# Kernel tuning notes

Measured on AMD Instinct MI355X. Metric: run time of the kernel, lower is better.

The kernel has to match this reference:

```python
import jax, jax.numpy as jnp
import numpy as np

B, OBS, ACT, NT, E, H1, H2, D = 4096, 390, 20, 10, 8, 1024, 512, 256


def setup_inputs() -> dict:
    key = jax.random.key(0)
    ks = jax.random.split(key, 16)
    f32 = jnp.float32

    def w(k, shape, fan_in):
        return jax.random.normal(k, shape, f32) / np.float32(np.sqrt(fan_in))

    return {
        "state_feat": jax.random.normal(ks[0], (B, OBS), f32),
        "act": jax.random.normal(ks[1], (B, ACT), f32),
        "task_id": jax.random.randint(ks[2], (B,), 0, NT, jnp.int32),
        "rep_W1": w(ks[3], (OBS + ACT, H1), OBS + ACT),
        "rep_b1": jnp.zeros((H1,), f32),
        "rep_W2": w(ks[4], (H1, H1), H1),
        "rep_b2": jnp.zeros((H1,), f32),
        "emb": 0.5 * jax.random.normal(ks[5], (NT, D), f32),
        "kW1": w(ks[6], (E, H1, H2), H1),
        "kb1": jnp.zeros((E, H2), f32),
        "kW2": w(ks[7], (E, H2, D), H2),
        "kb2": jnp.zeros((E, D), f32),
        "vW1": w(ks[8], (E, H1, H2), H1),
        "vb1": jnp.zeros((E, H2), f32),
        "vW2": w(ks[9], (E, H2, D), H2),
        "vb2": jnp.zeros((E, D), f32),
        "tW1": w(ks[10], (D, D), D),
        "tb1": jnp.zeros((D,), f32),
        "tW2": w(ks[11], (D, D), D),
        "tb2": jnp.zeros((D,), f32),
        "tW3": w(ks[12], (D, 1), D),
        "tb3": jnp.zeros((1,), f32),
    }


def reference(state_feat, act, task_id, rep_W1, rep_b1, rep_W2, rep_b2, emb,
              kW1, kb1, kW2, kb2, vW1, vb1, vW2, vb2,
              tW1, tb1, tW2, tb2, tW3, tb3):
    # representation: mlp([obs+act, 1024, 1024]) -> ReLU on first layer only
    x = jnp.concatenate([state_feat, act], axis=-1)              # [B, 410]
    rep = jnp.maximum(x @ rep_W1 + rep_b1, 0.0) @ rep_W2 + rep_b2  # [B, H1]
    query = jnp.tanh(emb[task_id])                               # [B, D]

    # batched per-expert key/value MLPs (grouped GEMM instead of python loop)
    hk = jnp.maximum(jnp.einsum('bi,eio->ebo', rep, kW1) + kb1[:, None, :], 0.0)
    keys = jnp.einsum('ebo,eod->ebd', hk, kW2) + kb2[:, None, :]   # [E, B, D]
    hv = jnp.maximum(jnp.einsum('bi,eio->ebo', rep, vW1) + vb1[:, None, :], 0.0)
    vals = jnp.einsum('ebo,eod->ebd', hv, vW2) + vb2[:, None, :]   # [E, B, D]

    scores = jnp.einsum('bd,ebd->be', query, keys)               # [B, E]
    weight = jax.nn.softmax(scores, axis=1)                      # [B, E]
    tower_in = jnp.einsum('be,ebd->bd', weight, vals)            # [B, D]

    # tower: mlp([256, 256, 256, 1]) -> ReLU, ReLU, Identity
    h = jnp.maximum(tower_in @ tW1 + tb1, 0.0)
    h = jnp.maximum(h @ tW2 + tb2, 0.0)
    q = (h @ tW3 + tb3)[:, 0]                                    # [B]

    expert_loss = -jnp.mean(
        jnp.sum(jnp.clip(jnp.log(weight + 1e-10), -6.0, 0.0), axis=-1) * 0.3)
    return q, expert_loss
```

## Files before the change

### kernel.cpp

```cpp
#include <hip/hip_runtime.h>

constexpr int Bn   = 4096;
constexpr int OBS  = 390;
constexpr int ACTN = 20;
constexpr int IN   = 410;
constexpr int KPAD = 416;
constexpr int E    = 8;
constexpr int NT   = 10;
constexpr int H1   = 1024;
constexpr int H2   = 512;
constexpr int D    = 256;

typedef __bf16 bf16x8 __attribute__((ext_vector_type(8)));
typedef float  f32x4  __attribute__((ext_vector_type(4)));

__device__ __forceinline__ unsigned short f2bf(float f) {
    unsigned int u = __float_as_uint(f);
    unsigned int r = u + 0x7fffu + ((u >> 16) & 1u);
    return (unsigned short)(r >> 16);
}
__device__ __forceinline__ float bf2f(unsigned short h) {
    return __uint_as_float(((unsigned int)h) << 16);
}
__device__ __forceinline__ void gload16(void* lds_dst, const void* g_src) {
    __builtin_amdgcn_global_load_lds(
        (const __attribute__((address_space(1))) void*)g_src,
        (__attribute__((address_space(3))) void*)lds_dst,
        16, 0, 0);
}

__global__ void prep_kernel(const float* __restrict__ sf, const float* __restrict__ ac,
                            unsigned short* __restrict__ x) {
    int idx = blockIdx.x * blockDim.x + threadIdx.x;
    if (idx >= Bn * KPAD) return;
    int b = idx / KPAD;
    int k = idx - b * KPAD;
    float v = 0.f;
    if (k < OBS) v = sf[b * OBS + k];
    else if (k < IN) v = ac[b * ACTN + (k - OBS)];
    x[idx] = f2bf(v);
}

__global__ __launch_bounds__(256) void qproj_kernel(
    const float* __restrict__ kW2, const float* __restrict__ kb2,
    const float* __restrict__ emb, float* __restrict__ qp, float* __restrict__ qb)
{
    __shared__ float tq[NT][D];
    for (int i = threadIdx.x; i < NT * D; i += 256)
        tq[i / D][i - (i / D) * D] = tanhf(emb[i]);
    __syncthreads();

    if (blockIdx.x < 16) {
        int e = blockIdx.x >> 1;
        int h = (blockIdx.x & 1) * 256 + threadIdx.x;
        const float4* row = (const float4*)(kW2 + ((long long)e * H2 + h) * D);
        float acc[NT] = {};
        for (int d4 = 0; d4 < D / 4; ++d4) {
            float4 wv = row[d4];
#pragma unroll
            for (int t = 0; t < NT; ++t)
                acc[t] += wv.x * tq[t][d4 * 4] + wv.y * tq[t][d4 * 4 + 1]
                        + wv.z * tq[t][d4 * 4 + 2] + wv.w * tq[t][d4 * 4 + 3];
        }
#pragma unroll
        for (int t = 0; t < NT; ++t)
            qp[((long long)e * NT + t) * H2 + h] = acc[t];
    } else {
        if (threadIdx.x < E * NT) {
            int e = threadIdx.x / NT, t = threadIdx.x - e * NT;
            float s = 0.f;
            for (int d = 0; d < D; ++d) s += kb2[e * D + d] * tq[t][d];
            qb[e * NT + t] = s;
        }
    }
}

struct TDesc {
    const float* W;
    unsigned short* WT;
    int K, N, Kpad;
    long long gsW, gsO;
    int tilesX, tilesY, perG;
    int start;
};
struct TDescArr { TDesc d[8]; };

__global__ __launch_bounds__(256) void mega_transpose(TDescArr da) {
    int bid = blockIdx.x;
    int i = 0;
#pragma unroll
    for (int j = 1; j < 8; ++j) if (bid >= da.d[j].start) i = j;
    TDesc dd = da.d[i];
    int local = bid - dd.start;
    int g   = local / dd.perG;
    int rem = local - g * dd.perG;
    int tyt = rem / dd.tilesX;
    int txt = rem - tyt * dd.tilesX;
    const float* W = dd.W + (long long)g * dd.gsW;
    unsigned short* WT = dd.WT + (long long)g * dd.gsO;

    __shared__ float tile[32][33];
    int tx = threadIdx.x & 31, ty = threadIdx.x >> 5;
    int k0 = tyt * 32, n0 = txt * 32;
#pragma unroll
    for (int r = 0; r < 4; ++r) {
        int k = k0 + ty + r * 8;
        tile[ty + r * 8][tx] = (k < dd.K) ? W[(long long)k * dd.N + n0 + tx] : 0.f;
    }
    __syncthreads();
#pragma unroll
    for (int r = 0; r < 4; ++r) {
        int n = n0 + ty + r * 8;
        WT[(long long)n * dd.Kpad + k0 + tx] = f2bf(tile[tx][ty + r * 8]);
    }
}

__global__ void bias_concat(const float* __restrict__ kb1, const float* __restrict__ vb1,
                            float* __restrict__ b1cat) {
    int i = blockIdx.x * blockDim.x + threadIdx.x;
    if (i < E * H2)          b1cat[i] = kb1[i];
    else if (i < 2 * E * H2) b1cat[i] = vb1[i - E * H2];
}

template <int ACTF, int OUTF, int BK>
__global__ __launch_bounds__(256) void gemm_bf16(
    const unsigned short* __restrict__ A, const unsigned short* __restrict__ BT,
    const float* __restrict__ bias, void* __restrict__ Cout,
    int K, int ldc,
    long long gsA, long long gsBT, long long gsBias, long long gsC)
{
    constexpr int CH   = BK / 8;
    constexpr int RPR  = 256 / CH;
    constexpr int RNDS = 128 / RPR;
    constexpr int TB   = 128 * BK * 2;
    constexpr int RS   = CH * 16;

    const int g = blockIdx.z;
    A    += (long long)g * gsA;
    BT   += (long long)g * gsBT;
    bias += (long long)g * gsBias;
    float*          Cf = (float*)Cout + (long long)g * gsC;
    unsigned short* Cb = (unsigned short*)Cout + (long long)g * gsC;

    __shared__ alignas(16) char smem[2 * TB];
    const int t  = threadIdx.x;
    const int w  = t >> 6, l = t & 63;
    const int lr = l & 15, lk = l >> 4;
    const int gm = blockIdx.y * 128, gn = blockIdx.x * 128;
    const int wm = (w >> 1) * 64,   wn = (w & 1) * 64;

    const int srow = t / CH;
    const int swzS = (CH == 8) ? (srow & 7) : ((srow >> 1) & 3);
    const int sc   = (t % CH) ^ swzS;
    const unsigned short* gA = A  + (long long)(gm + srow) * K + sc * 8;
    const unsigned short* gB = BT + (long long)(gn + srow) * K + sc * 8;

    const int swzL = (CH == 8) ? (lr & 7) : ((lr >> 1) & 3);
    const int aoff = (wm + lr) * RS + ((lk ^ swzL) * 16);
    const int boff = TB + (wn + lr) * RS + ((lk ^ swzL) * 16);

    f32x4 acc[4][4] = {};

    for (int k0 = 0; k0 < K; k0 += BK) {
#pragma unroll
        for (int j = 0; j < RNDS; ++j) {
            gload16(smem + j * 4096 + w * 1024,      gA + k0 + (long long)j * RPR * K);
            gload16(smem + TB + j * 4096 + w * 1024, gB + k0 + (long long)j * RPR * K);
        }
        __syncthreads();

        bf16x8 af[4], bfr[4];
#pragma unroll
        for (int i = 0; i < 4; ++i) {
            af[i]  = *(const bf16x8*)(smem + aoff + i * 16 * RS);
            bfr[i] = *(const bf16x8*)(smem + boff + i * 16 * RS);
        }
#pragma unroll
        for (int mi = 0; mi < 4; ++mi)
#pragma unroll
            for (int ni = 0; ni < 4; ++ni)
                acc[mi][ni] = __builtin_amdgcn_mfma_f32_16x16x32_bf16(
                    af[mi], bfr[ni], acc[mi][ni], 0, 0, 0);

        if constexpr (BK == 64) {
#pragma unroll
            for (int i = 0; i < 4; ++i) {
                af[i]  = *(const bf16x8*)(smem + (aoff ^ 64) + i * 16 * RS);
                bfr[i] = *(const bf16x8*)(smem + (boff ^ 64) + i * 16 * RS);
            }
#pragma unroll
            for (int mi = 0; mi < 4; ++mi)
#pragma unroll
                for (int ni = 0; ni < 4; ++ni)
                    acc[mi][ni] = __builtin_amdgcn_mfma_f32_16x16x32_bf16(
                        af[mi], bfr[ni], acc[mi][ni], 0, 0, 0);
        }
        __syncthreads();
    }

    const int orow0 = gm + wm + lk * 4;
    const int ocol0 = gn + wn + lr;
    float bv[4];
#pragma unroll
    for (int ni = 0; ni < 4; ++ni) bv[ni] = bias[gn + wn + lr + ni * 16];
#pragma unroll
    for (int mi = 0; mi < 4; ++mi)
#pragma unroll
        for (int ni = 0; ni < 4; ++ni)
#pragma unroll
            for (int r = 0; r < 4; ++r) {
                float v = acc[mi][ni][r] + bv[ni];
                if (ACTF == 1) v = fmaxf(v, 0.f);
                long long off = (long long)(orow0 + mi * 16 + r) * ldc + ocol0 + ni * 16;
                if (OUTF == 0) Cf[off] = v;
                else           Cb[off] = f2bf(v);
            }
}

template <int KTOT, int ACTF, int OUTF>
__global__ __launch_bounds__(512, 2) void gemm256(
    const unsigned short* __restrict__ A, const unsigned short* __restrict__ BT,
    const float* __restrict__ bias, void* __restrict__ Cout,
    int ldc, long long gsA, long long gsBT, long long gsBias, long long gsC)
{
    constexpr int NT_ = KTOT / 64;
    static_assert(NT_ >= 4 && (NT_ % 2) == 0, "KTOT must be multiple of 128");

    const int g = blockIdx.z;
    A    += (long long)g * gsA;
    BT   += (long long)g * gsBT;
    bias += (long long)g * gsBias;
    float*          Cf = (float*)Cout + (long long)g * gsC;
    unsigned short* Cb = (unsigned short*)Cout + (long long)g * gsC;

    __shared__ __align__(16) char smem[131072];

    const int tid = threadIdx.x;
    const int l  = tid & 63;
    const int lr = l & 15, lk = l >> 4;
    const int w  = tid >> 6;
    const int wr = w >> 2, wc = w & 3;
    const int gm = blockIdx.y * 256, gn = blockIdx.x * 256;

    const int srow = tid >> 3;
    const int cg   = (tid & 7) ^ (srow & 7);
    const unsigned short* gA = A  + (long long)(gm + srow) * KTOT + cg * 8;
    const unsigned short* gB = BT + (long long)(gn + srow) * KTOT + cg * 8;
    const int wbase = (tid & ~63) * 16;

    const int cs0 = ((0 | lk) ^ (lr & 7)) * 16;
    const int cs1 = ((4 | lk) ^ (lr & 7)) * 16;
    const int aRow = wr * 16384 + lr * 128;
    const int bRow = 32768 + (wc >> 1) * 16384 + ((wc & 1) * 64 + lr) * 128;

    f32x4 acc[8][4] = {};

    auto stA = [&](int c, int s, int kt) {
        const unsigned short* src = gA + (long long)(s * 128) * KTOT + kt * 64;
        char* d = smem + c * 65536 + s * 16384 + wbase;
        gload16(d,        src);
        gload16(d + 8192, src + (long long)64 * KTOT);
    };
    auto stB = [&](int c, int s, int kt) {
        const unsigned short* src = gB + (long long)(s * 128) * KTOT + kt * 64;
        char* d = smem + c * 65536 + 32768 + s * 16384 + wbase;
        gload16(d,        src);
        gload16(d + 8192, src + (long long)64 * KTOT);
    };

    stA(0, 0, 0); stA(0, 1, 0); stB(0, 0, 0); stB(0, 1, 0);
    stA(1, 0, 1); stA(1, 1, 1);
    asm volatile("s_waitcnt vmcnt(4)" ::: "memory");
    __builtin_amdgcn_s_barrier();
    __builtin_amdgcn_sched_barrier(0);

#pragma unroll
    for (int kt = 0; kt < NT_; ++kt) {
        const int c = kt & 1;
        const char* bufc = smem + c * 65536;
        bf16x8 a0[4], a1[4], b0[4], b1[4];

#pragma unroll
        for (int m = 0; m < 4; ++m) {
            const char* base = bufc + aRow + m * (16 * 128);
            a0[m] = *(const bf16x8*)(base + cs0);
            a1[m] = *(const bf16x8*)(base + cs1);
        }
#pragma unroll
        for (int n = 0; n < 4; ++n) {
            const char* base = bufc + bRow + n * (16 * 128);
            b0[n] = *(const bf16x8*)(base + cs0);
            b1[n] = *(const bf16x8*)(base + cs1);
        }
        if (kt + 1 < NT_) { stB(c ^ 1, 0, kt + 1); stB(c ^ 1, 1, kt + 1); }
        __builtin_amdgcn_s_setprio(1);
#pragma unroll
        for (int m = 0; m < 4; ++m)
#pragma unroll
            for (int n = 0; n < 4; ++n) {
                acc[m][n] = __builtin_amdgcn_mfma_f32_16x16x32_bf16(a0[m], b0[n], acc[m][n], 0, 0, 0);
                acc[m][n] = __builtin_amdgcn_mfma_f32_16x16x32_bf16(a1[m], b1[n], acc[m][n], 0, 0, 0);
            }
        __builtin_amdgcn_s_setprio(0);

#pragma unroll
        for (int m = 0; m < 4; ++m) {
            const char* base = bufc + aRow + (64 + m * 16) * 128;
            a0[m] = *(const bf16x8*)(base + cs0);
            a1[m] = *(const bf16x8*)(base + cs1);
        }
        asm volatile("s_waitcnt lgkmcnt(0)" ::: "memory");
        __builtin_amdgcn_sched_barrier(0);
        if (kt + 2 < NT_) {
            __builtin_amdgcn_s_barrier();
            __builtin_amdgcn_sched_barrier(0);
            stA(c, 0, kt + 2); stA(c, 1, kt + 2);
        }
        __builtin_amdgcn_s_setprio(1);
#pragma unroll
        for (int m = 0; m < 4; ++m)
#pragma unroll
            for (int n = 0; n < 4; ++n) {
                acc[4 + m][n] = __builtin_amdgcn_mfma_f32_16x16x32_bf16(a0[m], b0[n], acc[4 + m][n], 0, 0, 0);
                acc[4 + m][n] = __builtin_amdgcn_mfma_f32_16x16x32_bf16(a1[m], b1[n], acc[4 + m][n], 0, 0, 0);
            }
        __builtin_amdgcn_s_setprio(0);

        if (kt + 1 < NT_) {
            if (kt + 2 < NT_) { asm volatile("s_waitcnt vmcnt(4)" ::: "memory"); }
            else              { asm volatile("s_waitcnt vmcnt(0)" ::: "memory"); }
            __builtin_amdgcn_sched_barrier(0);
            __builtin_amdgcn_s_barrier();
            __builtin_amdgcn_sched_barrier(0);
        }
    }

    const int orow0 = gm + wr * 128 + lk * 4;
    const int ocol0 = gn + wc * 64 + lr;
    float bv[4];
#pragma unroll
    for (int ni = 0; ni < 4; ++ni) bv[ni] = bias[gn + wc * 64 + lr + ni * 16];
#pragma unroll
    for (int mi = 0; mi < 8; ++mi)
#pragma unroll
        for (int ni = 0; ni < 4; ++ni)
#pragma unroll
            for (int r = 0; r < 4; ++r) {
                float v = acc[mi][ni][r] + bv[ni];
                if (ACTF == 1) v = fmaxf(v, 0.f);
                long long off = (long long)(orow0 + mi * 16 + r) * ldc + ocol0 + ni * 16;
                if (OUTF == 0) Cf[off] = v;
                else           Cb[off] = f2bf(v);
            }
}

__global__ __launch_bounds__(256) void attn_score_kernel(
    const unsigned short* __restrict__ hk, const unsigned short* __restrict__ vals,
    const float* __restrict__ qp, const float* __restrict__ qb,
    const int* __restrict__ task_id, unsigned short* __restrict__ tower_in,
    float* __restrict__ loss_partial)
{
    int wv   = threadIdx.x >> 6;
    int lane = threadIdx.x & 63;
    int b    = blockIdx.x * 4 + wv;
    int t    = task_id[b];

    float s[E];
#pragma unroll
    for (int e = 0; e < E; ++e) {
        const ushort4 h4a = *(const ushort4*)&hk[((long long)e * Bn + b) * H2 + lane * 8];
        const ushort4 h4b = *(const ushort4*)&hk[((long long)e * Bn + b) * H2 + lane * 8 + 4];
        const float4 q4a = *(const float4*)&qp[((long long)e * NT + t) * H2 + lane * 8];
        const float4 q4b = *(const float4*)&qp[((long long)e * NT + t) * H2 + lane * 8 + 4];
        float p = bf2f(h4a.x) * q4a.x + bf2f(h4a.y) * q4a.y
                + bf2f(h4a.z) * q4a.z + bf2f(h4a.w) * q4a.w
                + bf2f(h4b.x) * q4b.x + bf2f(h4b.y) * q4b.y
                + bf2f(h4b.z) * q4b.z + bf2f(h4b.w) * q4b.w;
#pragma unroll
        for (int off = 32; off > 0; off >>= 1) p += __shfl_xor(p, off, 64);
        s[e] = p + qb[e * NT + t];
    }

    float m = s[0];
#pragma unroll
    for (int e = 1; e < E; ++e) m = fmaxf(m, s[e]);
    float wgt[E];
    float sum = 0.f;
#pragma unroll
    for (int e = 0; e < E; ++e) { wgt[e] = expf(s[e] - m); sum += wgt[e]; }
    float inv = 1.f / sum;

    int d0 = lane * 4;
    float4 acc = make_float4(0.f, 0.f, 0.f, 0.f);
    float lb = 0.f;
#pragma unroll
    for (int e = 0; e < E; ++e) {
        float we = wgt[e] * inv;
        uint2 vv = *(const uint2*)&vals[((long long)e * Bn + b) * D + d0];
        acc.x += we * __uint_as_float(vv.x << 16);
        acc.y += we * __uint_as_float(vv.x & 0xffff0000u);
        acc.z += we * __uint_as_float(vv.y << 16);
        acc.w += we * __uint_as_float(vv.y & 0xffff0000u);
        lb += fminf(fmaxf(logf(we + 1e-10f), -6.f), 0.f);
    }
    ushort4 o;
    o.x = f2bf(acc.x); o.y = f2bf(acc.y); o.z = f2bf(acc.z); o.w = f2bf(acc.w);
    *(ushort4*)&tower_in[(long long)b * D + d0] = o;

    __shared__ float sm[4];
    if (lane == 0) sm[wv] = lb;
    __syncthreads();
    if (threadIdx.x == 0)
        loss_partial[blockIdx.x] = sm[0] + sm[1] + sm[2] + sm[3];
}

__global__ __launch_bounds__(256) void qdot_loss_kernel(
    const float* __restrict__ t2, const float* __restrict__ tW3,
    const float* __restrict__ tb3, float* __restrict__ out,
    const float* __restrict__ lossp)
{
    if (blockIdx.x == Bn / 4) {
        float s = 0.f;
        for (int i = threadIdx.x; i < Bn / 4; i += 256) s += lossp[i];
#pragma unroll
        for (int off = 32; off > 0; off >>= 1) s += __shfl_xor(s, off, 64);
        __shared__ float sm[4];
        if ((threadIdx.x & 63) == 0) sm[threadIdx.x >> 6] = s;
        __syncthreads();
        if (threadIdx.x == 0) out[Bn] = (-0.3f / Bn) * (sm[0] + sm[1] + sm[2] + sm[3]);
        return;
    }
    int wv   = threadIdx.x >> 6;
    int lane = threadIdx.x & 63;
    int b    = blockIdx.x * 4 + wv;
    int d0   = lane * 4;
    float4 h4 = *(const float4*)&t2[(long long)b * D + d0];
    float4 w4 = *(const float4*)&tW3[d0];
    float p = h4.x * w4.x + h4.y * w4.y + h4.z * w4.z + h4.w * w4.w;
#pragma unroll
    for (int off = 32; off > 0; off >>= 1) p += __shfl_xor(p, off, 64);
    if (lane == 0) out[b] = p + tb3[0];
}

extern "C" void kernel_launch(void* const* d_in, const int* in_sizes, int n_in,
                              void* d_out, int out_size, void* d_ws, size_t ws_size,
                              hipStream_t stream) {
    const float* state_feat = (const float*)d_in[0];
    const float* act        = (const float*)d_in[1];
    const int*   task_id    = (const int*)d_in[2];
    const float* rep_W1 = (const float*)d_in[3];
    const float* rep_b1 = (const float*)d_in[4];
    const float* rep_W2 = (const float*)d_in[5];
    const float* rep_b2 = (const float*)d_in[6];
    const float* emb    = (const float*)d_in[7];
    const float* kW1 = (const float*)d_in[8];
    const float* kb1 = (const float*)d_in[9];
    const float* kW2 = (const float*)d_in[10];
    const float* kb2 = (const float*)d_in[11];
    const float* vW1 = (const float*)d_in[12];
    const float* vb1 = (const float*)d_in[13];
    const float* vW2 = (const float*)d_in[14];
    const float* vb2 = (const float*)d_in[15];
    const float* tW1 = (const float*)d_in[16];
    const float* tb1 = (const float*)d_in[17];
    const float* tW2 = (const float*)d_in[18];
    const float* tb2 = (const float*)d_in[19];
    const float* tW3 = (const float*)d_in[20];
    const float* tb3 = (const float*)d_in[21];
    float* out = (float*)d_out;

    char* p = (char*)d_ws;
    auto alloc = [&](size_t bytes) {
        char* r = p;
        p += (bytes + 255) & ~(size_t)255;
        return r;
    };
    unsigned short* x      = (unsigned short*)alloc((size_t)Bn * KPAD * 2);
    unsigned short* repW1T = (unsigned short*)alloc((size_t)H1 * KPAD * 2);
    unsigned short* repW2T = (unsigned short*)alloc((size_t)H1 * H1 * 2);
    unsigned short* w1T    = (unsigned short*)alloc((size_t)2 * E * H2 * H1 * 2);
    unsigned short* w2T    = (unsigned short*)alloc((size_t)E * D * H2 * 2);
    unsigned short* tW1T   = (unsigned short*)alloc((size_t)D * D * 2);
    unsigned short* tW2T   = (unsigned short*)alloc((size_t)D * D * 2);
    float*          b1cat  = (float*)alloc((size_t)2 * E * H2 * 4);
    float*          qp     = (float*)alloc((size_t)E * NT * H2 * 4);
    float*          qb     = (float*)alloc((size_t)E * NT * 4);
    char*           h1zone = alloc((size_t)Bn * H1 * 2);
    unsigned short* rep    = (unsigned short*)alloc((size_t)Bn * H1 * 2);
    unsigned short* hkv    = (unsigned short*)alloc((size_t)2 * E * Bn * H2 * 2);
    unsigned short* vals   = (unsigned short*)alloc((size_t)E * Bn * D * 2);
    float*          lossp  = (float*)alloc((size_t)(Bn / 4) * 4);

    unsigned short* h1       = (unsigned short*)h1zone;
    unsigned short* tower_in = (unsigned short*)h1zone;
    unsigned short* t1       = (unsigned short*)(h1zone + (size_t)Bn * D * 2);
    float*          t2       = (float*)(h1zone + (size_t)2 * Bn * D * 2);
    unsigned short* hk = hkv;
    unsigned short* hv = hkv + (size_t)E * Bn * H2;

    TDescArr da;
    int startAcc = 0;
    auto setd = [&](int i, const float* W, unsigned short* WT, int K, int N, int Kpad,
                    long long gsW, long long gsO, int groups) {
        TDesc& dd = da.d[i];
        dd.W = W; dd.WT = WT; dd.K = K; dd.N = N; dd.Kpad = Kpad;
        dd.gsW = gsW; dd.gsO = gsO;
        dd.tilesX = N / 32; dd.tilesY = Kpad / 32;
        dd.perG = dd.tilesX * dd.tilesY;
        dd.start = startAcc;
        startAcc += dd.perG * groups;
    };
    setd(0, rep_W1, repW1T, IN, H1, KPAD, 0, 0, 1);
    setd(1, rep_W2, repW2T, H1, H1, H1, 0, 0, 1);
    setd(2, kW1, w1T,                       H1, H2, H1, (long long)H1 * H2, (long long)H2 * H1, E);
    setd(3, vW1, w1T + (size_t)E * H2 * H1, H1, H2, H1, (long long)H1 * H2, (long long)H2 * H1, E);
    setd(4, vW2, w2T,                       H2, D, H2, (long long)H2 * D, (long long)D * H2, E);
    setd(5, tW1, tW1T, D, D, D, 0, 0, 1);
    setd(6, tW2, tW2T, D, D, D, 0, 0, 1);
    da.d[7] = da.d[6];
    da.d[7].start = 0x7fffffff;
    mega_transpose<<<startAcc, 256, 0, stream>>>(da);

    bias_concat<<<(2 * E * H2) / 256, 256, 0, stream>>>(kb1, vb1, b1cat);
    prep_kernel<<<(Bn * KPAD + 255) / 256, 256, 0, stream>>>(state_feat, act, x);
    qproj_kernel<<<17, 256, 0, stream>>>(kW2, kb2, emb, qp, qb);

    gemm_bf16<1, 1, 32><<<dim3(H1 / 128, Bn / 128, 1), 256, 0, stream>>>(
        x, repW1T, rep_b1, h1, KPAD, H1, 0, 0, 0, 0);
    gemm_bf16<0, 1, 64><<<dim3(H1 / 128, Bn / 128, 1), 256, 0, stream>>>(
        h1, repW2T, rep_b2, rep, H1, H1, 0, 0, 0, 0);

    gemm256<H1, 1, 1><<<dim3(H2 / 256, Bn / 256, 2 * E), 512, 0, stream>>>(
        rep, w1T, b1cat, hkv, H2,
        0, (long long)H2 * H1, H2, (long long)Bn * H2);
    gemm_bf16<0, 1, 64><<<dim3(D / 128, Bn / 128, E), 256, 0, stream>>>(
        hv, w2T, vb2, vals, H2, D,
        (long long)Bn * H2, (long long)D * H2, D, (long long)Bn * D);

    attn_score_kernel<<<Bn / 4, 256, 0, stream>>>(
        hk, vals, qp, qb, task_id, tower_in, lossp);

    gemm_bf16<1, 1, 64><<<dim3(D / 128, Bn / 128, 1), 256, 0, stream>>>(
        tower_in, tW1T, tb1, t1, D, D, 0, 0, 0, 0);
    gemm_bf16<1, 0, 64><<<dim3(D / 128, Bn / 128, 1), 256, 0, stream>>>(
        t1, tW2T, tb2, t2, D, D, 0, 0, 0, 0);

    qdot_loss_kernel<<<Bn / 4 + 1, 256, 0, stream>>>(t2, tW3, tb3, out, lossp);
}
```

Baseline: 188.4 us.

## Fuse key-score dot into expert GEMM epilogue, merge prep kernels, widen transpose

The expert layer-1 GEMM epilogue now dots the ReLU'd key hidden activations with the projected query for each row's task. It writes per-block partial scores to a small buffer instead of storing the bf16 hidden keys, and the attention kernel just sums these partials. This removes the write and re-read of the hk activations. The three small setup kernels are merged into one launch, and weight transposes use 64x64 tiles with float4 loads and 16-byte bf16 stores. In exchange the epilogue does extra gathered qp loads and shuffles, and scores are now computed from fp32 rather than bf16-rounded activations.

```diff
diff --git a/kernel.cpp b/kernel.cpp
--- a/kernel.cpp
+++ b/kernel.cpp
@@ -13,6 +13,7 @@
 
 typedef __bf16 bf16x8 __attribute__((ext_vector_type(8)));
 typedef float  f32x4  __attribute__((ext_vector_type(4)));
+typedef unsigned short u16x8 __attribute__((ext_vector_type(8)));
 
 __device__ __forceinline__ unsigned short f2bf(float f) {
     unsigned int u = __float_as_uint(f);
@@ -29,97 +30,110 @@
         16, 0, 0);
 }
 
-__global__ void prep_kernel(const float* __restrict__ sf, const float* __restrict__ ac,
-                            unsigned short* __restrict__ x) {
-    int idx = blockIdx.x * blockDim.x + threadIdx.x;
-    if (idx >= Bn * KPAD) return;
-    int b = idx / KPAD;
-    int k = idx - b * KPAD;
-    float v = 0.f;
-    if (k < OBS) v = sf[b * OBS + k];
-    else if (k < IN) v = ac[b * ACTN + (k - OBS)];
-    x[idx] = f2bf(v);
-}
-
-__global__ __launch_bounds__(256) void qproj_kernel(
+struct TD2 {
+    const float* W;
+    unsigned short* WT;
+    int K, Kpad, N;
+    long long gsW, gsO;
+    int tilesN, perG, start;
+};
+struct TD2Arr { TD2 d[8]; };
+
+__global__ __launch_bounds__(256) void tc64(TD2Arr da) {
+    int bid = blockIdx.x;
+    int i = 0;
+#pragma unroll
+    for (int j = 1; j < 8; ++j) if (bid >= da.d[j].start) i = j;
+    TD2 dd = da.d[i];
+    int local = bid - dd.start;
+    int g   = local / dd.perG;
+    int rem = local - g * dd.perG;
+    int kt  = rem / dd.tilesN;
+    int nt  = rem - kt * dd.tilesN;
+    const float* W = dd.W + (long long)g * dd.gsW;
+    unsigned short* WT = dd.WT + (long long)g * dd.gsO;
+    int k0 = kt * 64, n0 = nt * 64;
+
+    __shared__ float tile[64][68];
+    int t = threadIdx.x;
+    {
+        int kl  = t >> 4;
+        int nl4 = (t & 15) * 4;
+#pragma unroll
+        for (int r = 0; r < 4; ++r) {
+            int k = k0 + kl + r * 16;
+            float4 v = make_float4(0.f, 0.f, 0.f, 0.f);
+            if (k < dd.K) v = *(const float4*)(W + (long long)k * dd.N + n0 + nl4);
+            *(float4*)&tile[kl + r * 16][nl4] = v;
+        }
+    }
+    __syncthreads();
+    int nl = t >> 2, kc = (t & 3) * 16;
+    if (k0 + kc < dd.Kpad) {
+        u16x8 o0, o1;
+#pragma unroll
+        for (int j = 0; j < 8; ++j) {
+            o0[j] = f2bf(tile[kc + j][nl]);
+            o1[j] = f2bf(tile[kc + 8 + j][nl]);
+        }
+        unsigned short* dst = WT + (long long)(n0 + nl) * dd.Kpad + k0 + kc;
+        *(u16x8*)dst       = o0;
+        *(u16x8*)(dst + 8) = o1;
+    }
+}
+
+constexpr int PREPB = (Bn * KPAD) / 256;
+
+__global__ __launch_bounds__(256) void misc_kernel(
+    const float* __restrict__ sf, const float* __restrict__ ac,
+    unsigned short* __restrict__ x,
     const float* __restrict__ kW2, const float* __restrict__ kb2,
-    const float* __restrict__ emb, float* __restrict__ qp, float* __restrict__ qb)
+    const float* __restrict__ emb, float* __restrict__ qp, float* __restrict__ qb,
+    const float* __restrict__ kb1, const float* __restrict__ vb1,
+    float* __restrict__ b1cat)
 {
-    __shared__ float tq[NT][D];
-    for (int i = threadIdx.x; i < NT * D; i += 256)
-        tq[i / D][i - (i / D) * D] = tanhf(emb[i]);
-    __syncthreads();
-
-    if (blockIdx.x < 16) {
-        int e = blockIdx.x >> 1;
-        int h = (blockIdx.x & 1) * 256 + threadIdx.x;
-        const float4* row = (const float4*)(kW2 + ((long long)e * H2 + h) * D);
-        float acc[NT] = {};
-        for (int d4 = 0; d4 < D / 4; ++d4) {
-            float4 wv = row[d4];
+    int bid = blockIdx.x;
+    if (bid < PREPB) {
+        int idx = bid * 256 + threadIdx.x;
+        int b = idx / KPAD;
+        int k = idx - b * KPAD;
+        float v = 0.f;
+        if (k < OBS) v = sf[b * OBS + k];
+        else if (k < IN) v = ac[b * ACTN + (k - OBS)];
+        x[idx] = f2bf(v);
+        return;
+    }
+    if (bid < PREPB + 17) {
+        int qbid = bid - PREPB;
+        __shared__ float tq[NT][D];
+        for (int i = threadIdx.x; i < NT * D; i += 256)
+            tq[i / D][i - (i / D) * D] = tanhf(emb[i]);
+        __syncthreads();
+        if (qbid < 16) {
+            int e = qbid >> 1;
+            int h = (qbid & 1) * 256 + threadIdx.x;
+            const float4* row = (const float4*)(kW2 + ((long long)e * H2 + h) * D);
+            float acc[NT] = {};
+            for (int d4 = 0; d4 < D / 4; ++d4) {
+                float4 wv = row[d4];
+#pragma unroll
+                for (int t = 0; t < NT; ++t)
+                    acc[t] += wv.x * tq[t][d4 * 4] + wv.y * tq[t][d4 * 4 + 1]
+                            + wv.z * tq[t][d4 * 4 + 2] + wv.w * tq[t][d4 * 4 + 3];
+            }
 #pragma unroll
             for (int t = 0; t < NT; ++t)
-                acc[t] += wv.x * tq[t][d4 * 4] + wv.y * tq[t][d4 * 4 + 1]
-                        + wv.z * tq[t][d4 * 4 + 2] + wv.w * tq[t][d4 * 4 + 3];
-        }
-#pragma unroll
-        for (int t = 0; t < NT; ++t)
-            qp[((long long)e * NT + t) * H2 + h] = acc[t];
-    } else {
-        if (threadIdx.x < E * NT) {
+                qp[((long long)e * NT + t) * H2 + h] = acc[t];
+        } else if (threadIdx.x < E * NT) {
             int e = threadIdx.x / NT, t = threadIdx.x - e * NT;
             float s = 0.f;
             for (int d = 0; d < D; ++d) s += kb2[e * D + d] * tq[t][d];
             qb[e * NT + t] = s;
         }
-    }
-}
-
-struct TDesc {
-    const float* W;
-    unsigned short* WT;
-    int K, N, Kpad;
-    long long gsW, gsO;
-    int tilesX, tilesY, perG;
-    int start;
-};
-struct TDescArr { TDesc d[8]; };
-
-__global__ __launch_bounds__(256) void mega_transpose(TDescArr da) {
-    int bid = blockIdx.x;
-    int i = 0;
-#pragma unroll
-    for (int j = 1; j < 8; ++j) if (bid >= da.d[j].start) i = j;
-    TDesc dd = da.d[i];
-    int local = bid - dd.start;
-    int g   = local / dd.perG;
-    int rem = local - g * dd.perG;
-    int tyt = rem / dd.tilesX;
-    int txt = rem - tyt * dd.tilesX;
-    const float* W = dd.W + (long long)g * dd.gsW;
-    unsigned short* WT = dd.WT + (long long)g * dd.gsO;
-
-    __shared__ float tile[32][33];
-    int tx = threadIdx.x & 31, ty = threadIdx.x >> 5;
-    int k0 = tyt * 32, n0 = txt * 32;
-#pragma unroll
-    for (int r = 0; r < 4; ++r) {
-        int k = k0 + ty + r * 8;
-        tile[ty + r * 8][tx] = (k < dd.K) ? W[(long long)k * dd.N + n0 + tx] : 0.f;
-    }
-    __syncthreads();
-#pragma unroll
-    for (int r = 0; r < 4; ++r) {
-        int n = n0 + ty + r * 8;
-        WT[(long long)n * dd.Kpad + k0 + tx] = f2bf(tile[tx][ty + r * 8]);
-    }
-}
-
-__global__ void bias_concat(const float* __restrict__ kb1, const float* __restrict__ vb1,
-                            float* __restrict__ b1cat) {
-    int i = blockIdx.x * blockDim.x + threadIdx.x;
-    if (i < E * H2)          b1cat[i] = kb1[i];
-    else if (i < 2 * E * H2) b1cat[i] = vb1[i - E * H2];
+        return;
+    }
+    int i = (bid - PREPB - 17) * 256 + threadIdx.x;
+    b1cat[i] = (i < E * H2) ? kb1[i] : vb1[i - E * H2];
 }
 
 template <int ACTF, int OUTF, int BK>
@@ -217,11 +231,13 @@
             }
 }
 
-template <int KTOT, int ACTF, int OUTF>
+template <int KTOT, int ACTF, int OUTF, int SC>
 __global__ __launch_bounds__(512, 2) void gemm256(
     const unsigned short* __restrict__ A, const unsigned short* __restrict__ BT,
     const float* __restrict__ bias, void* __restrict__ Cout,
-    int ldc, long long gsA, long long gsBT, long long gsBias, long long gsC)
+    int ldc, long long gsA, long long gsBT, long long gsBias, long long gsC,
+    const int* __restrict__ task_id, const float* __restrict__ qp,
+    float* __restrict__ spart)
 {
     constexpr int NT_ = KTOT / 64;
     static_assert(NT_ >= 4 && (NT_ % 2) == 0, "KTOT must be multiple of 128");
@@ -340,25 +356,51 @@
     float bv[4];
 #pragma unroll
     for (int ni = 0; ni < 4; ++ni) bv[ni] = bias[gn + wc * 64 + lr + ni * 16];
-#pragma unroll
-    for (int mi = 0; mi < 8; ++mi)
-#pragma unroll
-        for (int ni = 0; ni < 4; ++ni)
+
+    if (SC && g < E) {
+#pragma unroll
+        for (int mi = 0; mi < 8; ++mi) {
+            int tr[4];
+#pragma unroll
+            for (int r = 0; r < 4; ++r) tr[r] = task_id[orow0 + mi * 16 + r];
 #pragma unroll
             for (int r = 0; r < 4; ++r) {
-                float v = acc[mi][ni][r] + bv[ni];
-                if (ACTF == 1) v = fmaxf(v, 0.f);
-                long long off = (long long)(orow0 + mi * 16 + r) * ldc + ocol0 + ni * 16;
-                if (OUTF == 0) Cf[off] = v;
-                else           Cb[off] = f2bf(v);
+                float rp = 0.f;
+#pragma unroll
+                for (int ni = 0; ni < 4; ++ni) {
+                    float v = acc[mi][ni][r] + bv[ni];
+                    v = fmaxf(v, 0.f);
+                    rp += v * qp[((long long)(g * NT + tr[r])) * H2 + ocol0 + ni * 16];
+                }
+                rp += __shfl_xor(rp, 1);
+                rp += __shfl_xor(rp, 2);
+                rp += __shfl_xor(rp, 4);
+                rp += __shfl_xor(rp, 8);
+                if (lr == 0)
+                    spart[(((long long)g * Bn + orow0 + mi * 16 + r) << 3)
+                          + (wc << 1) + blockIdx.x] = rp;
             }
-}
-
-__global__ __launch_bounds__(256) void attn_score_kernel(
-    const unsigned short* __restrict__ hk, const unsigned short* __restrict__ vals,
-    const float* __restrict__ qp, const float* __restrict__ qb,
-    const int* __restrict__ task_id, unsigned short* __restrict__ tower_in,
-    float* __restrict__ loss_partial)
+        }
+    } else {
+#pragma unroll
+        for (int mi = 0; mi < 8; ++mi)
+#pragma unroll
+            for (int ni = 0; ni < 4; ++ni)
+#pragma unroll
+                for (int r = 0; r < 4; ++r) {
+                    float v = acc[mi][ni][r] + bv[ni];
+                    if (ACTF == 1) v = fmaxf(v, 0.f);
+                    long long off = (long long)(orow0 + mi * 16 + r) * ldc + ocol0 + ni * 16;
+                    if (OUTF == 0) Cf[off] = v;
+                    else           Cb[off] = f2bf(v);
+                }
+    }
+}
+
+__global__ __launch_bounds__(256) void attn_kernel(
+    const float* __restrict__ spart, const float* __restrict__ qb,
+    const int* __restrict__ task_id, const unsigned short* __restrict__ vals,
+    unsigned short* __restrict__ tower_in, float* __restrict__ loss_partial)
 {
     int wv   = threadIdx.x >> 6;
     int lane = threadIdx.x & 63;
@@ -368,17 +410,9 @@
     float s[E];
 #pragma unroll
     for (int e = 0; e < E; ++e) {
-        const ushort4 h4a = *(const ushort4*)&hk[((long long)e * Bn + b) * H2 + lane * 8];
-        const ushort4 h4b = *(const ushort4*)&hk[((long long)e * Bn + b) * H2 + lane * 8 + 4];
-        const float4 q4a = *(const float4*)&qp[((long long)e * NT + t) * H2 + lane * 8];
-        const float4 q4b = *(const float4*)&qp[((long long)e * NT + t) * H2 + lane * 8 + 4];
-        float p = bf2f(h4a.x) * q4a.x + bf2f(h4a.y) * q4a.y
-                + bf2f(h4a.z) * q4a.z + bf2f(h4a.w) * q4a.w
-                + bf2f(h4b.x) * q4b.x + bf2f(h4b.y) * q4b.y
-                + bf2f(h4b.z) * q4b.z + bf2f(h4b.w) * q4b.w;
-#pragma unroll
-        for (int off = 32; off > 0; off >>= 1) p += __shfl_xor(p, off, 64);
-        s[e] = p + qb[e * NT + t];
+        const float4* sp = (const float4*)(spart + (((long long)e * Bn + b) << 3));
+        float4 p0 = sp[0], p1 = sp[1];
+        s[e] = p0.x + p0.y + p0.z + p0.w + p1.x + p1.y + p1.z + p1.w + qb[e * NT + t];
     }
 
     float m = s[0];
@@ -489,56 +523,56 @@
     unsigned short* rep    = (unsigned short*)alloc((size_t)Bn * H1 * 2);
     unsigned short* hkv    = (unsigned short*)alloc((size_t)2 * E * Bn * H2 * 2);
     unsigned short* vals   = (unsigned short*)alloc((size_t)E * Bn * D * 2);
+    float*          spart  = (float*)alloc((size_t)E * Bn * 8 * 4);
     float*          lossp  = (float*)alloc((size_t)(Bn / 4) * 4);
 
     unsigned short* h1       = (unsigned short*)h1zone;
     unsigned short* tower_in = (unsigned short*)h1zone;
     unsigned short* t1       = (unsigned short*)(h1zone + (size_t)Bn * D * 2);
     float*          t2       = (float*)(h1zone + (size_t)2 * Bn * D * 2);
-    unsigned short* hk = hkv;
     unsigned short* hv = hkv + (size_t)E * Bn * H2;
 
-    TDescArr da;
+    TD2Arr da;
     int startAcc = 0;
-    auto setd = [&](int i, const float* W, unsigned short* WT, int K, int N, int Kpad,
+    auto setd = [&](int i, const float* W, unsigned short* WT, int K, int Kpad, int N,
                     long long gsW, long long gsO, int groups) {
-        TDesc& dd = da.d[i];
-        dd.W = W; dd.WT = WT; dd.K = K; dd.N = N; dd.Kpad = Kpad;
+        TD2& dd = da.d[i];
+        dd.W = W; dd.WT = WT; dd.K = K; dd.Kpad = Kpad; dd.N = N;
         dd.gsW = gsW; dd.gsO = gsO;
-        dd.tilesX = N / 32; dd.tilesY = Kpad / 32;
-        dd.perG = dd.tilesX * dd.tilesY;
+        dd.tilesN = N / 64;
+        dd.perG = ((Kpad + 63) / 64) * dd.tilesN;
         dd.start = startAcc;
         startAcc += dd.perG * groups;
     };
-    setd(0, rep_W1, repW1T, IN, H1, KPAD, 0, 0, 1);
+    setd(0, rep_W1, repW1T, IN, KPAD, H1, 0, 0, 1);
     setd(1, rep_W2, repW2T, H1, H1, H1, 0, 0, 1);
-    setd(2, kW1, w1T,                       H1, H2, H1, (long long)H1 * H2, (long long)H2 * H1, E);
-    setd(3, vW1, w1T + (size_t)E * H2 * H1, H1, H2, H1, (long long)H1 * H2, (long long)H2 * H1, E);
-    setd(4, vW2, w2T,                       H2, D, H2, (long long)H2 * D, (long long)D * H2, E);
+    setd(2, kW1, w1T,                       H1, H1, H2, (long long)H1 * H2, (long long)H2 * H1, E);
+    setd(3, vW1, w1T + (size_t)E * H2 * H1, H1, H1, H2, (long long)H1 * H2, (long long)H2 * H1, E);
+    setd(4, vW2, w2T,                       H2, H2, D, (long long)H2 * D, (long long)D * H2, E);
     setd(5, tW1, tW1T, D, D, D, 0, 0, 1);
     setd(6, tW2, tW2T, D, D, D, 0, 0, 1);
     da.d[7] = da.d[6];
     da.d[7].start = 0x7fffffff;
-    mega_transpose<<<startAcc, 256, 0, stream>>>(da);
-
-    bias_concat<<<(2 * E * H2) / 256, 256, 0, stream>>>(kb1, vb1, b1cat);
-    prep_kernel<<<(Bn * KPAD + 255) / 256, 256, 0, stream>>>(state_feat, act, x);
-    qproj_kernel<<<17, 256, 0, stream>>>(kW2, kb2, emb, qp, qb);
+    tc64<<<startAcc, 256, 0, stream>>>(da);
+
+    misc_kernel<<<PREPB + 17 + 32, 256, 0, stream>>>(
+        state_feat, act, x, kW2, kb2, emb, qp, qb, kb1, vb1, b1cat);
 
     gemm_bf16<1, 1, 32><<<dim3(H1 / 128, Bn / 128, 1), 256, 0, stream>>>(
         x, repW1T, rep_b1, h1, KPAD, H1, 0, 0, 0, 0);
     gemm_bf16<0, 1, 64><<<dim3(H1 / 128, Bn / 128, 1), 256, 0, stream>>>(
         h1, repW2T, rep_b2, rep, H1, H1, 0, 0, 0, 0);
 
-    gemm256<H1, 1, 1><<<dim3(H2 / 256, Bn / 256, 2 * E), 512, 0, stream>>>(
+    gemm256<H1, 1, 1, 1><<<dim3(H2 / 256, Bn / 256, 2 * E), 512, 0, stream>>>(
         rep, w1T, b1cat, hkv, H2,
-        0, (long long)H2 * H1, H2, (long long)Bn * H2);
+        0, (long long)H2 * H1, H2, (long long)Bn * H2,
+        task_id, qp, spart);
     gemm_bf16<0, 1, 64><<<dim3(D / 128, Bn / 128, E), 256, 0, stream>>>(
         hv, w2T, vb2, vals, H2, D,
         (long long)Bn * H2, (long long)D * H2, D, (long long)Bn * D);
 
-    attn_score_kernel<<<Bn / 4, 256, 0, stream>>>(
-        hk, vals, qp, qb, task_id, tower_in, lossp);
+    attn_kernel<<<Bn / 4, 256, 0, stream>>>(
+        spart, qb, task_id, vals, tower_in, lossp);
 
     gemm_bf16<1, 1, 64><<<dim3(D / 128, Bn / 128, 1), 256, 0, stream>>>(
         tower_in, tW1T, tb1, t1, D, D, 0, 0, 0, 0);
```

Measured after the change: 181.3 us. 1.04x faster.
